# Optimization experiments

Hardware: AMD Instinct MI355X
Metric: run time of the kernel (lower is better)

## Reference

```python
import jax, jax.numpy as jnp
import numpy as np

B, C, H, W = 8, 256, 64, 64


def setup_inputs() -> dict:
    key = jax.random.key(0)
    ks = jax.random.split(key, 9)
    s = 1.0 / np.sqrt(C)  # conv2d default init scale
    return {
        "foreground": jax.random.normal(ks[0], (B, C, H, W), jnp.float32),
        "background": jax.random.normal(ks[1], (B, C, H, W), jnp.float32),
        "mask": jax.random.uniform(ks[2], (B, C, H, W), jnp.float32),
        "Wq": jax.random.normal(ks[3], (C, C), jnp.float32) * s,
        "bq": jnp.zeros((C,), jnp.float32),
        "Wk": jax.random.normal(ks[4], (C, C), jnp.float32) * s,
        "bk": jnp.zeros((C,), jnp.float32),
        "Wv": jax.random.normal(ks[5], (C, C), jnp.float32) * s,
        "bv": jnp.zeros((C,), jnp.float32),
        "gamma": jnp.ones((1,), jnp.float32),
    }


def _conv1x1(x, Wt, b):
    # 1x1 conv == per-pixel channel matmul; x: [B,C,H,W], Wt: [Cout,Cin]
    return jnp.einsum('bchw,oc->bohw', x, Wt) + b[None, :, None, None]


def reference(foreground, background, mask, Wq, bq, Wk, bk, Wv, bv, gamma):
    b, c, h, w = foreground.shape
    hw = h * w
    # mask is already at feature resolution (interpolate would be identity)
    q = _conv1x1(foreground, Wq, bq).reshape(b, c, hw)   # [B,C,HW]
    k = _conv1x1(background, Wk, bk).reshape(b, c, hw)   # [B,C,HW]
    # bmm(q, k^T): channel-channel correlation [B,C,C]
    corr = jnp.einsum('bci,bdi->bcd', q, k)
    m_r = mask.reshape(b, c, hw)                          # [B,C,HW]
    # bmm(corr, m_r): mask-modulated scores [B,C,HW]
    scores = jnp.einsum('bcd,bdi->bci', corr, m_r)
    energy = jax.nn.softmax(scores, axis=-1)
    v = _conv1x1(foreground, Wv, bv).reshape(b, c, hw)
    attended = (energy * v).reshape(b, c, h, w)
    out = foreground * mask + gamma[0] * (1.0 - mask) * attended
    return out
```

## Files before the change

### kernel.cpp

```cpp
#include <hip/hip_runtime.h>
#include <math.h>

#define B_    8
#define C_    256
#define HW_   4096
#define CHW_  ((long)C_ * HW_)

#define BKT   32
#define LDH   40
#define LDI   132
#define KS    16
#define KCH   (HW_ / KS)

typedef __attribute__((ext_vector_type(8))) short bf16x8;
typedef __attribute__((ext_vector_type(4))) float f32x4;
#define MFMA_BF16(a, b, c) __builtin_amdgcn_mfma_f32_16x16x32_bf16((a), (b), (c), 0, 0, 0)

union frag_u { uint4 u4; bf16x8 bf; };

__device__ __forceinline__ void cvt_hl4(const float4 f, uint* h, uint* l) {
    uint u0 = __float_as_uint(f.x), u1 = __float_as_uint(f.y),
         u2 = __float_as_uint(f.z), u3 = __float_as_uint(f.w);
    uint h0 = (u0 + 0x8000u) & 0xFFFF0000u, h1 = (u1 + 0x8000u) & 0xFFFF0000u,
         h2 = (u2 + 0x8000u) & 0xFFFF0000u, h3 = (u3 + 0x8000u) & 0xFFFF0000u;
    h[0] = (h0 >> 16) | h1;
    h[1] = (h2 >> 16) | h3;
    float l0 = f.x - __uint_as_float(h0), l1 = f.y - __uint_as_float(h1),
          l2 = f.z - __uint_as_float(h2), l3 = f.w - __uint_as_float(h3);
    uint a0 = __float_as_uint(l0) & 0xFFFF0000u, a1 = __float_as_uint(l1) & 0xFFFF0000u,
         a2 = __float_as_uint(l2) & 0xFFFF0000u, a3 = __float_as_uint(l3) & 0xFFFF0000u;
    l[0] = (a0 >> 16) | a1;
    l[1] = (a2 >> 16) | a3;
}
__device__ __forceinline__ void cvt_h4(const float4 f, uint* h) {
    uint u0 = __float_as_uint(f.x), u1 = __float_as_uint(f.y),
         u2 = __float_as_uint(f.z), u3 = __float_as_uint(f.w);
    uint h0 = (u0 + 0x8000u) & 0xFFFF0000u, h1 = (u1 + 0x8000u) & 0xFFFF0000u,
         h2 = (u2 + 0x8000u) & 0xFFFF0000u, h3 = (u3 + 0x8000u) & 0xFFFF0000u;
    h[0] = (h0 >> 16) | h1;
    h[1] = (h2 >> 16) | h3;
}

__device__ __forceinline__ void cvt8_hl(const float* f, bf16x8* bh, bf16x8* bl) {
    frag_u H, L;
    uint hw[8];
    #pragma unroll
    for (int j = 0; j < 4; ++j) {
        uint u0 = __float_as_uint(f[2*j]), u1 = __float_as_uint(f[2*j+1]);
        uint h0 = (u0 + 0x8000u) & 0xFFFF0000u;
        uint h1 = (u1 + 0x8000u) & 0xFFFF0000u;
        ((uint*)&H.u4)[j] = (h0 >> 16) | h1;
        hw[2*j] = h0; hw[2*j+1] = h1;
    }
    #pragma unroll
    for (int j = 0; j < 4; ++j) {
        float l0 = f[2*j]   - __uint_as_float(hw[2*j]);
        float l1 = f[2*j+1] - __uint_as_float(hw[2*j+1]);
        ((uint*)&L.u4)[j] = ((__float_as_uint(l0) & 0xFFFF0000u) >> 16)
                          |  (__float_as_uint(l1) & 0xFFFF0000u);
    }
    *bh = H.bf; *bl = L.bf;
}
__device__ __forceinline__ void cvt8_h(const float* f, bf16x8* bh) {
    frag_u H;
    #pragma unroll
    for (int j = 0; j < 4; ++j) {
        uint h0 = (__float_as_uint(f[2*j])   + 0x8000u) & 0xFFFF0000u;
        uint h1 = (__float_as_uint(f[2*j+1]) + 0x8000u) & 0xFFFF0000u;
        ((uint*)&H.u4)[j] = (h0 >> 16) | h1;
    }
    *bh = H.bf;
}

__global__ __launch_bounds__(256) void conv_w(
    const float* __restrict__ Wv, ushort* __restrict__ Wvh)
{
    const int i = (blockIdx.x * 256 + threadIdx.x) * 4;
    float4 v = *reinterpret_cast<const float4*>(&Wv[i]);
    uint h[2];
    cvt_h4(v, h);
    *reinterpret_cast<uint2*>(&Wvh[i]) = make_uint2(h[0], h[1]);
}

__global__ __launch_bounds__(256, 3) void gemm_nt_mfma(
    const float* __restrict__ F, const float* __restrict__ G,
    float* __restrict__ part,
    float* __restrict__ fsum, float* __restrict__ gsum)
{
    __shared__ ushort Ah[128 * LDH], Al[128 * LDH], Bh[128 * LDH], Bl[128 * LDH];

    const int z  = blockIdx.z;
    const int b  = z >> 4;
    const int ks = z & (KS - 1);
    const int c0 = blockIdx.y * 128;
    const int d0 = blockIdx.x * 128;
    const float* Fb = F + (long)b * CHW_ + (long)ks * KCH;
    const float* Gb = G + (long)b * CHW_ + (long)ks * KCH;
    const bool doF = (blockIdx.x == 0);
    const bool doG = (blockIdx.y == 0);

    const int t    = threadIdx.x;
    const int srow = t & 127;
    const int skf  = (t >> 7) * 16;
    const int lane = t & 63, w = t >> 6;
    const int col  = lane & 15, quad = lane >> 4;
    const int wm   = (w >> 1) * 64, wn = (w & 1) * 64;

    f32x4 acc[4][4] = {};
    float rsF = 0.0f, rsG = 0.0f;

    for (int kt = 0; kt < KCH; kt += BKT) {
        {
            const float* s = &Fb[(long)(c0 + srow) * HW_ + kt + skf];
            float4 v0 = *reinterpret_cast<const float4*>(s);
            float4 v1 = *reinterpret_cast<const float4*>(s + 4);
            float4 v2 = *reinterpret_cast<const float4*>(s + 8);
            float4 v3 = *reinterpret_cast<const float4*>(s + 12);
            if (doF) {
                rsF += (v0.x + v0.y + v0.z + v0.w) + (v1.x + v1.y + v1.z + v1.w)
                     + (v2.x + v2.y + v2.z + v2.w) + (v3.x + v3.y + v3.z + v3.w);
            }
            uint h[4], l[4];
            cvt_hl4(v0, h + 0, l + 0);
            cvt_hl4(v1, h + 2, l + 2);
            *reinterpret_cast<uint4*>(&Ah[srow * LDH + skf]) = make_uint4(h[0], h[1], h[2], h[3]);
            *reinterpret_cast<uint4*>(&Al[srow * LDH + skf]) = make_uint4(l[0], l[1], l[2], l[3]);
            cvt_hl4(v2, h + 0, l + 0);
            cvt_hl4(v3, h + 2, l + 2);
            *reinterpret_cast<uint4*>(&Ah[srow * LDH + skf + 8]) = make_uint4(h[0], h[1], h[2], h[3]);
            *reinterpret_cast<uint4*>(&Al[srow * LDH + skf + 8]) = make_uint4(l[0], l[1], l[2], l[3]);
        }
        {
            const float* s = &Gb[(long)(d0 + srow) * HW_ + kt + skf];
            float4 v0 = *reinterpret_cast<const float4*>(s);
            float4 v1 = *reinterpret_cast<const float4*>(s + 4);
            float4 v2 = *reinterpret_cast<const float4*>(s + 8);
            float4 v3 = *reinterpret_cast<const float4*>(s + 12);
            if (doG) {
                rsG += (v0.x + v0.y + v0.z + v0.w) + (v1.x + v1.y + v1.z + v1.w)
                     + (v2.x + v2.y + v2.z + v2.w) + (v3.x + v3.y + v3.z + v3.w);
            }
            uint h[4], l[4];
            cvt_hl4(v0, h + 0, l + 0);
            cvt_hl4(v1, h + 2, l + 2);
            *reinterpret_cast<uint4*>(&Bh[srow * LDH + skf]) = make_uint4(h[0], h[1], h[2], h[3]);
            *reinterpret_cast<uint4*>(&Bl[srow * LDH + skf]) = make_uint4(l[0], l[1], l[2], l[3]);
            cvt_hl4(v2, h + 0, l + 0);
            cvt_hl4(v3, h + 2, l + 2);
            *reinterpret_cast<uint4*>(&Bh[srow * LDH + skf + 8]) = make_uint4(h[0], h[1], h[2], h[3]);
            *reinterpret_cast<uint4*>(&Bl[srow * LDH + skf + 8]) = make_uint4(l[0], l[1], l[2], l[3]);
        }
        __syncthreads();

        bf16x8 bfh[4], bfl[4];
        #pragma unroll
        for (int tj = 0; tj < 4; ++tj) {
            const int r = (wn + tj * 16 + col) * LDH + quad * 8;
            bfh[tj] = *reinterpret_cast<const bf16x8*>(&Bh[r]);
            bfl[tj] = *reinterpret_cast<const bf16x8*>(&Bl[r]);
        }
        #pragma unroll
        for (int ti = 0; ti < 4; ++ti) {
            const int r = (wm + ti * 16 + col) * LDH + quad * 8;
            bf16x8 afh = *reinterpret_cast<const bf16x8*>(&Ah[r]);
            bf16x8 afl = *reinterpret_cast<const bf16x8*>(&Al[r]);
            #pragma unroll
            for (int tj = 0; tj < 4; ++tj) {
                acc[ti][tj] = MFMA_BF16(afh, bfh[tj], acc[ti][tj]);
                acc[ti][tj] = MFMA_BF16(afh, bfl[tj], acc[ti][tj]);
                acc[ti][tj] = MFMA_BF16(afl, bfh[tj], acc[ti][tj]);
            }
        }
        __syncthreads();
    }

    if (doF) atomicAdd(&fsum[b * C_ + c0 + srow], rsF);
    if (doG) atomicAdd(&gsum[b * C_ + d0 + srow], rsG);

    float* P = part + (long)z * C_ * C_;
    #pragma unroll
    for (int ti = 0; ti < 4; ++ti) {
        const int m = c0 + wm + ti * 16 + quad * 4;
        #pragma unroll
        for (int tj = 0; tj < 4; ++tj) {
            const int n = d0 + wn + tj * 16 + col;
            #pragma unroll
            for (int r = 0; r < 4; ++r)
                P[(long)(m + r) * C_ + n] = acc[ti][tj][r];
        }
    }
}

__global__ __launch_bounds__(256, 3) void gemm_stats_mfma(
    const ushort* __restrict__ corrh, const ushort* __restrict__ corrl,
    const float* __restrict__ mask,
    float* __restrict__ pmax, float* __restrict__ psum)
{
    __shared__ float Ms[32 * LDI];
    __shared__ float pm[2][128], ps[2][128];

    const int b  = blockIdx.z;
    const int m0 = blockIdx.y * 128;
    const int n0 = blockIdx.x * 128;
    const ushort* Ahb = corrh + (long)b * C_ * C_;
    const ushort* Alb = corrl + (long)b * C_ * C_;
    const float*  Mb  = mask + (long)b * CHW_;

    const int t    = threadIdx.x;
    const int se   = t >> 3;
    const int si4  = (t & 7) * 4;
    const int lane = t & 63, w = t >> 6;
    const int col  = lane & 15, quad = lane >> 4;
    const int wm   = (w >> 1) * 64, wn = (w & 1) * 64;

    f32x4 acc[4][4] = {};

    for (int kt = 0; kt < C_; kt += BKT) {
        __syncthreads();
        #pragma unroll
        for (int rep = 0; rep < 4; ++rep) {
            const int i = rep * 32 + si4;
            float4 v = *reinterpret_cast<const float4*>(&Mb[(long)(kt + se) * HW_ + n0 + i]);
            *reinterpret_cast<float4*>(&Ms[se * LDI + i]) = v;
        }
        __syncthreads();

        bf16x8 ah[4], al[4];
        #pragma unroll
        for (int ti = 0; ti < 4; ++ti) {
            const long oa = (long)(m0 + wm + ti * 16 + col) * C_ + kt + quad * 8;
            ah[ti] = *reinterpret_cast<const bf16x8*>(&Ahb[oa]);
            al[ti] = *reinterpret_cast<const bf16x8*>(&Alb[oa]);
        }
        #pragma unroll
        for (int tj = 0; tj < 4; ++tj) {
            const int i = wn + tj * 16 + col;
            float fv[8];
            #pragma unroll
            for (int j = 0; j < 8; ++j)
                fv[j] = Ms[(quad * 8 + j) * LDI + i];
            bf16x8 bh, bl;
            cvt8_hl(fv, &bh, &bl);
            #pragma unroll
            for (int ti = 0; ti < 4; ++ti) {
                acc[ti][tj] = MFMA_BF16(ah[ti], bh, acc[ti][tj]);
                acc[ti][tj] = MFMA_BF16(ah[ti], bl, acc[ti][tj]);
                acc[ti][tj] = MFMA_BF16(al[ti], bh, acc[ti][tj]);
            }
        }
    }

    #pragma unroll
    for (int ti = 0; ti < 4; ++ti) {
        #pragma unroll
        for (int r = 0; r < 4; ++r) {
            float mx = fmaxf(fmaxf(acc[ti][0][r], acc[ti][1][r]),
                             fmaxf(acc[ti][2][r], acc[ti][3][r]));
            mx = fmaxf(mx, __shfl_xor(mx, 1));
            mx = fmaxf(mx, __shfl_xor(mx, 2));
            mx = fmaxf(mx, __shfl_xor(mx, 4));
            mx = fmaxf(mx, __shfl_xor(mx, 8));
            float se2 = __expf(acc[ti][0][r] - mx) + __expf(acc[ti][1][r] - mx)
                      + __expf(acc[ti][2][r] - mx) + __expf(acc[ti][3][r] - mx);
            se2 += __shfl_xor(se2, 1);
            se2 += __shfl_xor(se2, 2);
            se2 += __shfl_xor(se2, 4);
            se2 += __shfl_xor(se2, 8);
            if (col == 0) {
                const int rb = wm + ti * 16 + quad * 4 + r;
                pm[w & 1][rb] = mx;
                ps[w & 1][rb] = se2;
            }
        }
    }
    __syncthreads();
    if (t < 128) {
        const float a0 = pm[0][t], a1 = pm[1][t];
        const float gm = fmaxf(a0, a1);
        const float gs = ps[0][t] * __expf(a0 - gm) + ps[1][t] * __expf(a1 - gm);
        const long rowg = (long)b * C_ + m0 + t;
        pmax[rowg * 32 + blockIdx.x] = gm;
        psum[rowg * 32 + blockIdx.x] = gs;
    }
}

__global__ __launch_bounds__(256, 2) void gemm_fused_final(
    const ushort* __restrict__ corrh, const ushort* __restrict__ corrl,
    const ushort* __restrict__ Wvh,
    const float* __restrict__ mask,   const float* __restrict__ fg,
    const float* __restrict__ pmax,   const float* __restrict__ psum,
    const float* __restrict__ bv,     const float* __restrict__ gamma,
    float* __restrict__ out)
{
    __shared__ float Ms[32 * LDI];
    __shared__ float Fs[32 * LDI];
    __shared__ float sm[128], si[128];

    const int b  = blockIdx.z;
    const int m0 = blockIdx.y * 128;
    const int n0 = blockIdx.x * 128;
    const ushort* Ahb = corrh + (long)b * C_ * C_;
    const ushort* Alb = corrl + (long)b * C_ * C_;
    const float*  Mb  = mask + (long)b * CHW_;
    const float*  Fgb = fg   + (long)b * CHW_;

    const int t    = threadIdx.x;
    const int se   = t >> 3;
    const int si4  = (t & 7) * 4;
    const int lane = t & 63, w = t >> 6;
    const int col  = lane & 15, quad = lane >> 4;
    const int wm   = (w >> 1) * 64, wn = (w & 1) * 64;

    if (t < 128) {
        const long rowg = (long)b * C_ + m0 + t;
        const float* pmr = pmax + rowg * 32;
        const float* psr = psum + rowg * 32;
        float gm = -INFINITY;
        #pragma unroll
        for (int i = 0; i < 32; ++i) gm = fmaxf(gm, pmr[i]);
        float gs = 0.0f;
        #pragma unroll
        for (int i = 0; i < 32; ++i) gs += psr[i] * __expf(pmr[i] - gm);
        sm[t] = gm;
        si[t] = 1.0f / gs;
    }

    f32x4 acc_s[4][4] = {};
    f32x4 acc_v[4][4] = {};

    for (int kt = 0; kt < C_; kt += BKT) {
        __syncthreads();
        #pragma unroll
        for (int rep = 0; rep < 4; ++rep) {
            const int i = rep * 32 + si4;
            float4 vm = *reinterpret_cast<const float4*>(&Mb[(long)(kt + se) * HW_ + n0 + i]);
            float4 vf = *reinterpret_cast<const float4*>(&Fgb[(long)(kt + se) * HW_ + n0 + i]);
            *reinterpret_cast<float4*>(&Ms[se * LDI + i]) = vm;
            *reinterpret_cast<float4*>(&Fs[se * LDI + i]) = vf;
        }
        __syncthreads();

        bf16x8 ah[4], al[4], aw[4];
        #pragma unroll
        for (int ti = 0; ti < 4; ++ti) {
            const long oa = (long)(m0 + wm + ti * 16 + col) * C_ + kt + quad * 8;
            ah[ti] = *reinterpret_cast<const bf16x8*>(&Ahb[oa]);
            al[ti] = *reinterpret_cast<const bf16x8*>(&Alb[oa]);
            aw[ti] = *reinterpret_cast<const bf16x8*>(&Wvh[oa]);
        }
        #pragma unroll
        for (int tj = 0; tj < 4; ++tj) {
            const int i = wn + tj * 16 + col;
            float fv[8], gv[8];
            #pragma unroll
            for (int j = 0; j < 8; ++j) {
                fv[j] = Ms[(quad * 8 + j) * LDI + i];
                gv[j] = Fs[(quad * 8 + j) * LDI + i];
            }
            bf16x8 bh, bl, bf;
            cvt8_hl(fv, &bh, &bl);
            cvt8_h(gv, &bf);
            #pragma unroll
            for (int ti = 0; ti < 4; ++ti) {
                acc_s[ti][tj] = MFMA_BF16(ah[ti], bh, acc_s[ti][tj]);
                acc_s[ti][tj] = MFMA_BF16(ah[ti], bl, acc_s[ti][tj]);
                acc_s[ti][tj] = MFMA_BF16(al[ti], bh, acc_s[ti][tj]);
                acc_v[ti][tj] = MFMA_BF16(aw[ti], bf, acc_v[ti][tj]);
            }
        }
    }

    const float g = gamma[0];
    #pragma unroll
    for (int ti = 0; ti < 4; ++ti) {
        #pragma unroll
        for (int r = 0; r < 4; ++r) {
            const int lrow = wm + ti * 16 + quad * 4 + r;
            const float mx  = sm[lrow];
            const float inv = si[lrow] * g;
            #pragma unroll
            for (int tj = 0; tj < 4; ++tj)
                acc_s[ti][tj][r] = __expf(acc_s[ti][tj][r] - mx) * inv;
        }
    }

    #pragma unroll
    for (int ti = 0; ti < 4; ++ti) {
        const int m = m0 + wm + ti * 16 + quad * 4;
        #pragma unroll
        for (int r = 0; r < 4; ++r) {
            const float bvm = bv[m + r];
            #pragma unroll
            for (int tj = 0; tj < 4; ++tj) {
                const int n = n0 + wn + tj * 16 + col;
                const long e = (long)b * CHW_ + (long)(m + r) * HW_ + n;
                const float f  = fg[e];
                const float mk = mask[e];
                const float vv = acc_v[ti][tj][r] + bvm;
                out[e] = f * mk + (1.0f - mk) * acc_s[ti][tj][r] * vv;
            }
        }
    }
}

__global__ __launch_bounds__(256) void reduce_part(
    const float* __restrict__ part, float* __restrict__ S1)
{
    const long idx = (long)blockIdx.x * 256 + threadIdx.x;
    const int  b   = (int)(idx >> 16);
    const long e   = idx & 65535;
    const float* p = part + ((long)b * KS) * 65536 + e;
    float s = 0.0f;
    #pragma unroll
    for (int ks = 0; ks < KS; ++ks) s += p[(long)ks * 65536];
    S1[idx] = s;
}

#define BK64 16
#define LDT64 68
__global__ __launch_bounds__(256) void gemm_nt64(
    const float* __restrict__ S1, const float* __restrict__ Wk,
    float* __restrict__ T)
{
    __shared__ float As[BK64][LDT64];
    __shared__ float Bs[BK64][LDT64];
    const int r0 = blockIdx.y * 64;
    const int d0 = blockIdx.x * 64;
    const int t   = threadIdx.x;
    const int tx  = t & 15, ty = t >> 4;
    const int tx4 = tx * 4, ty4 = ty * 4;
    const int am  = t >> 2, ak4 = (t & 3) * 4;

    float acc[4][4] = {};
    for (int k0 = 0; k0 < C_; k0 += BK64) {
        float4 av = *reinterpret_cast<const float4*>(&S1[(long)(r0 + am) * C_ + k0 + ak4]);
        float4 bw = *reinterpret_cast<const float4*>(&Wk[(long)(d0 + am) * C_ + k0 + ak4]);
        As[ak4+0][am]=av.x; As[ak4+1][am]=av.y; As[ak4+2][am]=av.z; As[ak4+3][am]=av.w;
        Bs[ak4+0][am]=bw.x; Bs[ak4+1][am]=bw.y; Bs[ak4+2][am]=bw.z; Bs[ak4+3][am]=bw.w;
        __syncthreads();
        #pragma unroll
        for (int kk = 0; kk < BK64; ++kk) {
            float4 a = *reinterpret_cast<const float4*>(&As[kk][ty4]);
            float4 x = *reinterpret_cast<const float4*>(&Bs[kk][tx4]);
            const float ar[4] = {a.x,a.y,a.z,a.w};
            const float xr[4] = {x.x,x.y,x.z,x.w};
            #pragma unroll
            for (int r = 0; r < 4; ++r)
                #pragma unroll
                for (int s = 0; s < 4; ++s)
                    acc[r][s] = fmaf(ar[r], xr[s], acc[r][s]);
        }
        __syncthreads();
    }
    #pragma unroll
    for (int r = 0; r < 4; ++r) {
        float4 o; o.x=acc[r][0]; o.y=acc[r][1]; o.z=acc[r][2]; o.w=acc[r][3];
        *reinterpret_cast<float4*>(&T[(long)(r0 + ty4 + r) * C_ + d0 + tx4]) = o;
    }
}

__global__ __launch_bounds__(256) void gemm_nn64_rank1(
    const float* __restrict__ Wq, const float* __restrict__ T,
    const float* __restrict__ Wk, const float* __restrict__ bk,
    const float* __restrict__ bq,
    const float* __restrict__ fsum, const float* __restrict__ gsum,
    ushort* __restrict__ corrh, ushort* __restrict__ corrl)
{
    __shared__ float As[BK64][LDT64];
    __shared__ float Bs[BK64][LDT64];
    __shared__ float u_s[64], wh_s[64];
    const int b  = blockIdx.z;
    const int m0 = blockIdx.y * 64;
    const int n0 = blockIdx.x * 64;
    const float* Tb = T + (long)b * C_ * C_;

    const int t   = threadIdx.x;
    const int tx  = t & 15, ty = t >> 4;
    const int tx4 = tx * 4, ty4 = ty * 4;
    const int am  = t >> 2, ak4 = (t & 3) * 4;
    const int xk  = ty,     xn4 = tx4;

    if (t < 64) {
        const float* wrow = Wq + (long)(m0 + t) * C_;
        const float* s = fsum + b * C_;
        float a = 0.0f;
        for (int e2 = 0; e2 < C_; ++e2) a = fmaf(wrow[e2], s[e2], a);
        u_s[t] = a;
    } else if (t < 128) {
        const int d = n0 + (t - 64);
        const float* wrow = Wk + (long)d * C_;
        const float* s = gsum + b * C_;
        float a = 0.0f;
        for (int e2 = 0; e2 < C_; ++e2) a = fmaf(wrow[e2], s[e2], a);
        wh_s[t - 64] = a + (float)HW_ * bk[d];
    }

    float acc[4][4] = {};
    for (int k0 = 0; k0 < C_; k0 += BK64) {
        float4 av = *reinterpret_cast<const float4*>(&Wq[(long)(m0 + am) * C_ + k0 + ak4]);
        float4 xv = *reinterpret_cast<const float4*>(&Tb[(long)(k0 + xk) * C_ + n0 + xn4]);
        As[ak4+0][am]=av.x; As[ak4+1][am]=av.y; As[ak4+2][am]=av.z; As[ak4+3][am]=av.w;
        *reinterpret_cast<float4*>(&Bs[xk][xn4]) = xv;
        __syncthreads();
        #pragma unroll
        for (int kk = 0; kk < BK64; ++kk) {
            float4 a = *reinterpret_cast<const float4*>(&As[kk][ty4]);
            float4 x = *reinterpret_cast<const float4*>(&Bs[kk][tx4]);
            const float ar[4] = {a.x,a.y,a.z,a.w};
            const float xr[4] = {x.x,x.y,x.z,x.w};
            #pragma unroll
            for (int r = 0; r < 4; ++r)
                #pragma unroll
                for (int s = 0; s < 4; ++s)
                    acc[r][s] = fmaf(ar[r], xr[s], acc[r][s]);
        }
        __syncthreads();
    }

    float4 bkv = *reinterpret_cast<const float4*>(&bk[n0 + tx4]);
    float4 whv = make_float4(wh_s[tx4], wh_s[tx4+1], wh_s[tx4+2], wh_s[tx4+3]);
    #pragma unroll
    for (int r = 0; r < 4; ++r) {
        const int m = m0 + ty4 + r;
        const float um = u_s[ty4 + r];
        const float bm = bq[m];
        float4 o;
        o.x = acc[r][0] + um*bkv.x + bm*whv.x;
        o.y = acc[r][1] + um*bkv.y + bm*whv.y;
        o.z = acc[r][2] + um*bkv.z + bm*whv.z;
        o.w = acc[r][3] + um*bkv.w + bm*whv.w;
        uint h[2], l[2];
        cvt_hl4(o, h, l);
        const long e = (long)b * C_ * C_ + (long)m * C_ + n0 + tx4;
        *reinterpret_cast<uint2*>(&corrh[e]) = make_uint2(h[0], h[1]);
        *reinterpret_cast<uint2*>(&corrl[e]) = make_uint2(l[0], l[1]);
    }
}

extern "C" void kernel_launch(void* const* d_in, const int* in_sizes, int n_in,
                              void* d_out, int out_size, void* d_ws, size_t ws_size,
                              hipStream_t stream)
{
    const float* fg    = (const float*)d_in[0];
    const float* bg    = (const float*)d_in[1];
    const float* mask  = (const float*)d_in[2];
    const float* Wq    = (const float*)d_in[3];
    const float* bq    = (const float*)d_in[4];
    const float* Wk    = (const float*)d_in[5];
    const float* bk    = (const float*)d_in[6];
    const float* Wv    = (const float*)d_in[7];
    const float* bv    = (const float*)d_in[8];
    const float* gamma = (const float*)d_in[9];
    float* out = (float*)d_out;

    char* ws = (char*)d_ws;
    float*  part   = (float*)(ws);
    float*  S1     = (float*)(ws + 33554432);
    float*  T      = (float*)(ws + 35651584);
    ushort* corrh  = (ushort*)(ws + 37748736);
    ushort* corrl  = (ushort*)(ws + 38797312);
    ushort* Wvh    = (ushort*)(ws + 39845888);
    float*  fsum   = (float*)(ws + 39976960);
    float*  gsum   = (float*)(ws + 39985152);
    float*  pmax   = (float*)(ws + 39993344);
    float*  psum   = (float*)(ws + 40255488);

    const dim3 blk(256);

    hipMemsetAsync(fsum, 0, 16384, stream);

    conv_w<<<dim3(64), blk, 0, stream>>>(Wv, Wvh);

    gemm_nt_mfma<<<dim3(2, 2, B_ * KS), blk, 0, stream>>>(fg, bg, part, fsum, gsum);
    reduce_part<<<dim3(B_ * C_ * C_ / 256), blk, 0, stream>>>(part, S1);

    gemm_nt64<<<dim3(C_ / 64, B_ * C_ / 64), blk, 0, stream>>>(S1, Wk, T);
    gemm_nn64_rank1<<<dim3(4, 4, B_), blk, 0, stream>>>(
        Wq, T, Wk, bk, bq, fsum, gsum, corrh, corrl);

    gemm_stats_mfma<<<dim3(HW_ / 128, C_ / 128, B_), blk, 0, stream>>>(
        corrh, corrl, mask, pmax, psum);

    gemm_fused_final<<<dim3(HW_ / 128, C_ / 128, B_), blk, 0, stream>>>(
        corrh, corrl, Wvh, mask, fg, pmax, psum, bv, gamma, out);
}
```

Measured before the change: 277.5 us.

## Pre-transpose and convert mask and foreground to split bf16 for direct MFMA loads

Adds a transpose_cvt kernel that writes mask (high and low bf16 parts) and foreground (high bf16 part) in a [B,HW,C] layout once. The stats and fused-final GEMMs then load MFMA B fragments straight from global memory instead of staging fp32 tiles in shared memory and converting them per block with barriers. This removes the repeated conversion and the LDS traffic from two kernels. In exchange it adds an extra pass that writes about 48MB of bf16 data, and the GEMMs now read uncached, strided global fragments without LDS reuse. The new buffers reuse the partial-sum workspace region.

```diff
diff --git a/kernel.cpp b/kernel.cpp
--- a/kernel.cpp
+++ b/kernel.cpp
@@ -8,7 +8,6 @@
 
 #define BKT   32
 #define LDH   40
-#define LDI   132
 #define KS    16
 #define KCH   (HW_ / KS)
 
@@ -41,35 +40,17 @@
     h[1] = (h2 >> 16) | h3;
 }
 
-__device__ __forceinline__ void cvt8_hl(const float* f, bf16x8* bh, bf16x8* bl) {
-    frag_u H, L;
-    uint hw[8];
-    #pragma unroll
-    for (int j = 0; j < 4; ++j) {
-        uint u0 = __float_as_uint(f[2*j]), u1 = __float_as_uint(f[2*j+1]);
-        uint h0 = (u0 + 0x8000u) & 0xFFFF0000u;
-        uint h1 = (u1 + 0x8000u) & 0xFFFF0000u;
-        ((uint*)&H.u4)[j] = (h0 >> 16) | h1;
-        hw[2*j] = h0; hw[2*j+1] = h1;
-    }
-    #pragma unroll
-    for (int j = 0; j < 4; ++j) {
-        float l0 = f[2*j]   - __uint_as_float(hw[2*j]);
-        float l1 = f[2*j+1] - __uint_as_float(hw[2*j+1]);
-        ((uint*)&L.u4)[j] = ((__float_as_uint(l0) & 0xFFFF0000u) >> 16)
-                          |  (__float_as_uint(l1) & 0xFFFF0000u);
-    }
-    *bh = H.bf; *bl = L.bf;
-}
-__device__ __forceinline__ void cvt8_h(const float* f, bf16x8* bh) {
-    frag_u H;
-    #pragma unroll
-    for (int j = 0; j < 4; ++j) {
-        uint h0 = (__float_as_uint(f[2*j])   + 0x8000u) & 0xFFFF0000u;
-        uint h1 = (__float_as_uint(f[2*j+1]) + 0x8000u) & 0xFFFF0000u;
-        ((uint*)&H.u4)[j] = (h0 >> 16) | h1;
-    }
-    *bh = H.bf;
+__device__ __forceinline__ void cvt2_hl(float a, float b2, uint* h, uint* l) {
+    uint ua = __float_as_uint(a), ub = __float_as_uint(b2);
+    uint ha = (ua + 0x8000u) & 0xFFFF0000u, hb = (ub + 0x8000u) & 0xFFFF0000u;
+    *h = (ha >> 16) | hb;
+    float la = a - __uint_as_float(ha), lb = b2 - __uint_as_float(hb);
+    *l = ((__float_as_uint(la) & 0xFFFF0000u) >> 16) | (__float_as_uint(lb) & 0xFFFF0000u);
+}
+__device__ __forceinline__ uint cvt2_h(float a, float b2) {
+    uint ha = (__float_as_uint(a) + 0x8000u) & 0xFFFF0000u;
+    uint hb = (__float_as_uint(b2) + 0x8000u) & 0xFFFF0000u;
+    return (ha >> 16) | hb;
 }
 
 __global__ __launch_bounds__(256) void conv_w(
@@ -80,6 +61,47 @@
     uint h[2];
     cvt_h4(v, h);
     *reinterpret_cast<uint2*>(&Wvh[i]) = make_uint2(h[0], h[1]);
+}
+
+__global__ __launch_bounds__(256) void transpose_cvt(
+    const float* __restrict__ mask, const float* __restrict__ fg,
+    ushort* __restrict__ mTh, ushort* __restrict__ mTl, ushort* __restrict__ fTh)
+{
+    __shared__ float Ms[64][65];
+    __shared__ float Fs[64][65];
+
+    const int b  = blockIdx.z;
+    const int c0 = blockIdx.y * 64;
+    const int i0 = blockIdx.x * 64;
+    const int t  = threadIdx.x;
+
+    const int lr = t >> 2;
+    const int lc = (t & 3) * 16;
+    const float* mp = mask + (long)b * CHW_ + (long)(c0 + lr) * HW_ + i0 + lc;
+    const float* fp = fg   + (long)b * CHW_ + (long)(c0 + lr) * HW_ + i0 + lc;
+    #pragma unroll
+    for (int j = 0; j < 16; j += 4) {
+        *reinterpret_cast<float4*>(&Ms[lr][lc + j]) = *reinterpret_cast<const float4*>(mp + j);
+        *reinterpret_cast<float4*>(&Fs[lr][lc + j]) = *reinterpret_cast<const float4*>(fp + j);
+    }
+    __syncthreads();
+
+    const int oi = t >> 2;
+    const int oc = (t & 3) * 16;
+    uint hm[8], lm[8], hf[8];
+    #pragma unroll
+    for (int j = 0; j < 8; ++j) {
+        const float m0v = Ms[oc + 2 * j][oi], m1v = Ms[oc + 2 * j + 1][oi];
+        cvt2_hl(m0v, m1v, &hm[j], &lm[j]);
+        hf[j] = cvt2_h(Fs[oc + 2 * j][oi], Fs[oc + 2 * j + 1][oi]);
+    }
+    const long ro = ((long)b * HW_ + i0 + oi) * C_ + c0 + oc;
+    *reinterpret_cast<uint4*>(&mTh[ro])     = make_uint4(hm[0], hm[1], hm[2], hm[3]);
+    *reinterpret_cast<uint4*>(&mTh[ro + 8]) = make_uint4(hm[4], hm[5], hm[6], hm[7]);
+    *reinterpret_cast<uint4*>(&mTl[ro])     = make_uint4(lm[0], lm[1], lm[2], lm[3]);
+    *reinterpret_cast<uint4*>(&mTl[ro + 8]) = make_uint4(lm[4], lm[5], lm[6], lm[7]);
+    *reinterpret_cast<uint4*>(&fTh[ro])     = make_uint4(hf[0], hf[1], hf[2], hf[3]);
+    *reinterpret_cast<uint4*>(&fTh[ro + 8]) = make_uint4(hf[4], hf[5], hf[6], hf[7]);
 }
 
 __global__ __launch_bounds__(256, 3) void gemm_nt_mfma(
@@ -191,12 +213,11 @@
     }
 }
 
-__global__ __launch_bounds__(256, 3) void gemm_stats_mfma(
+__global__ __launch_bounds__(256, 2) void gemm_stats_mfma(
     const ushort* __restrict__ corrh, const ushort* __restrict__ corrl,
-    const float* __restrict__ mask,
+    const ushort* __restrict__ mTh,   const ushort* __restrict__ mTl,
     float* __restrict__ pmax, float* __restrict__ psum)
 {
-    __shared__ float Ms[32 * LDI];
     __shared__ float pm[2][128], ps[2][128];
 
     const int b  = blockIdx.z;
@@ -204,28 +225,19 @@
     const int n0 = blockIdx.x * 128;
     const ushort* Ahb = corrh + (long)b * C_ * C_;
     const ushort* Alb = corrl + (long)b * C_ * C_;
-    const float*  Mb  = mask + (long)b * CHW_;
+    const ushort* Bhb = mTh + (long)b * HW_ * C_;
+    const ushort* Blb = mTl + (long)b * HW_ * C_;
 
     const int t    = threadIdx.x;
-    const int se   = t >> 3;
-    const int si4  = (t & 7) * 4;
     const int lane = t & 63, w = t >> 6;
     const int col  = lane & 15, quad = lane >> 4;
     const int wm   = (w >> 1) * 64, wn = (w & 1) * 64;
 
     f32x4 acc[4][4] = {};
 
+    #pragma unroll 1
     for (int kt = 0; kt < C_; kt += BKT) {
-        __syncthreads();
-        #pragma unroll
-        for (int rep = 0; rep < 4; ++rep) {
-            const int i = rep * 32 + si4;
-            float4 v = *reinterpret_cast<const float4*>(&Mb[(long)(kt + se) * HW_ + n0 + i]);
-            *reinterpret_cast<float4*>(&Ms[se * LDI + i]) = v;
-        }
-        __syncthreads();
-
-        bf16x8 ah[4], al[4];
+        bf16x8 ah[4], al[4], bh[4], bl[4];
         #pragma unroll
         for (int ti = 0; ti < 4; ++ti) {
             const long oa = (long)(m0 + wm + ti * 16 + col) * C_ + kt + quad * 8;
@@ -234,18 +246,17 @@
         }
         #pragma unroll
         for (int tj = 0; tj < 4; ++tj) {
-            const int i = wn + tj * 16 + col;
-            float fv[8];
-            #pragma unroll
-            for (int j = 0; j < 8; ++j)
-                fv[j] = Ms[(quad * 8 + j) * LDI + i];
-            bf16x8 bh, bl;
-            cvt8_hl(fv, &bh, &bl);
+            const long ob = (long)(n0 + wn + tj * 16 + col) * C_ + kt + quad * 8;
+            bh[tj] = *reinterpret_cast<const bf16x8*>(&Bhb[ob]);
+            bl[tj] = *reinterpret_cast<const bf16x8*>(&Blb[ob]);
+        }
+        #pragma unroll
+        for (int tj = 0; tj < 4; ++tj) {
             #pragma unroll
             for (int ti = 0; ti < 4; ++ti) {
-                acc[ti][tj] = MFMA_BF16(ah[ti], bh, acc[ti][tj]);
-                acc[ti][tj] = MFMA_BF16(ah[ti], bl, acc[ti][tj]);
-                acc[ti][tj] = MFMA_BF16(al[ti], bh, acc[ti][tj]);
+                acc[ti][tj] = MFMA_BF16(ah[ti], bh[tj], acc[ti][tj]);
+                acc[ti][tj] = MFMA_BF16(ah[ti], bl[tj], acc[ti][tj]);
+                acc[ti][tj] = MFMA_BF16(al[ti], bh[tj], acc[ti][tj]);
             }
         }
     }
@@ -287,13 +298,13 @@
 __global__ __launch_bounds__(256, 2) void gemm_fused_final(
     const ushort* __restrict__ corrh, const ushort* __restrict__ corrl,
     const ushort* __restrict__ Wvh,
+    const ushort* __restrict__ mTh,   const ushort* __restrict__ mTl,
+    const ushort* __restrict__ fTh,
     const float* __restrict__ mask,   const float* __restrict__ fg,
     const float* __restrict__ pmax,   const float* __restrict__ psum,
     const float* __restrict__ bv,     const float* __restrict__ gamma,
     float* __restrict__ out)
 {
-    __shared__ float Ms[32 * LDI];
-    __shared__ float Fs[32 * LDI];
     __shared__ float sm[128], si[128];
 
     const int b  = blockIdx.z;
@@ -301,12 +312,11 @@
     const int n0 = blockIdx.x * 128;
     const ushort* Ahb = corrh + (long)b * C_ * C_;
     const ushort* Alb = corrl + (long)b * C_ * C_;
-    const float*  Mb  = mask + (long)b * CHW_;
-    const float*  Fgb = fg   + (long)b * CHW_;
+    const ushort* Bhb = mTh + (long)b * HW_ * C_;
+    const ushort* Blb = mTl + (long)b * HW_ * C_;
+    const ushort* Bfb = fTh + (long)b * HW_ * C_;
 
     const int t    = threadIdx.x;
-    const int se   = t >> 3;
-    const int si4  = (t & 7) * 4;
     const int lane = t & 63, w = t >> 6;
     const int col  = lane & 15, quad = lane >> 4;
     const int wm   = (w >> 1) * 64, wn = (w & 1) * 64;
@@ -328,19 +338,9 @@
     f32x4 acc_s[4][4] = {};
     f32x4 acc_v[4][4] = {};
 
+    #pragma unroll 1
     for (int kt = 0; kt < C_; kt += BKT) {
-        __syncthreads();
-        #pragma unroll
-        for (int rep = 0; rep < 4; ++rep) {
-            const int i = rep * 32 + si4;
-            float4 vm = *reinterpret_cast<const float4*>(&Mb[(long)(kt + se) * HW_ + n0 + i]);
-            float4 vf = *reinterpret_cast<const float4*>(&Fgb[(long)(kt + se) * HW_ + n0 + i]);
-            *reinterpret_cast<float4*>(&Ms[se * LDI + i]) = vm;
-            *reinterpret_cast<float4*>(&Fs[se * LDI + i]) = vf;
-        }
-        __syncthreads();
-
-        bf16x8 ah[4], al[4], aw[4];
+        bf16x8 ah[4], al[4], aw[4], bh[4], bl[4], bf[4];
         #pragma unroll
         for (int ti = 0; ti < 4; ++ti) {
             const long oa = (long)(m0 + wm + ti * 16 + col) * C_ + kt + quad * 8;
@@ -350,25 +350,24 @@
         }
         #pragma unroll
         for (int tj = 0; tj < 4; ++tj) {
-            const int i = wn + tj * 16 + col;
-            float fv[8], gv[8];
-            #pragma unroll
-            for (int j = 0; j < 8; ++j) {
-                fv[j] = Ms[(quad * 8 + j) * LDI + i];
-                gv[j] = Fs[(quad * 8 + j) * LDI + i];
-            }
-            bf16x8 bh, bl, bf;
-            cvt8_hl(fv, &bh, &bl);
-            cvt8_h(gv, &bf);
+            const long ob = (long)(n0 + wn + tj * 16 + col) * C_ + kt + quad * 8;
+            bh[tj] = *reinterpret_cast<const bf16x8*>(&Bhb[ob]);
+            bl[tj] = *reinterpret_cast<const bf16x8*>(&Blb[ob]);
+            bf[tj] = *reinterpret_cast<const bf16x8*>(&Bfb[ob]);
+        }
+        #pragma unroll
+        for (int tj = 0; tj < 4; ++tj) {
             #pragma unroll
             for (int ti = 0; ti < 4; ++ti) {
-                acc_s[ti][tj] = MFMA_BF16(ah[ti], bh, acc_s[ti][tj]);
-                acc_s[ti][tj] = MFMA_BF16(ah[ti], bl, acc_s[ti][tj]);
-                acc_s[ti][tj] = MFMA_BF16(al[ti], bh, acc_s[ti][tj]);
-                acc_v[ti][tj] = MFMA_BF16(aw[ti], bf, acc_v[ti][tj]);
-            }
-        }
-    }
+                acc_s[ti][tj] = MFMA_BF16(ah[ti], bh[tj], acc_s[ti][tj]);
+                acc_s[ti][tj] = MFMA_BF16(ah[ti], bl[tj], acc_s[ti][tj]);
+                acc_s[ti][tj] = MFMA_BF16(al[ti], bh[tj], acc_s[ti][tj]);
+                acc_v[ti][tj] = MFMA_BF16(aw[ti], bf[tj], acc_v[ti][tj]);
+            }
+        }
+    }
+
+    __syncthreads();
 
     const float g = gamma[0];
     #pragma unroll
@@ -564,6 +563,9 @@
     float*  gsum   = (float*)(ws + 39985152);
     float*  pmax   = (float*)(ws + 39993344);
     float*  psum   = (float*)(ws + 40255488);
+    ushort* mTh    = (ushort*)(ws);
+    ushort* mTl    = (ushort*)(ws + 16777216);
+    ushort* fTh    = (ushort*)(ws + 40517632);
 
     const dim3 blk(256);
 
@@ -573,14 +575,17 @@
 
     gemm_nt_mfma<<<dim3(2, 2, B_ * KS), blk, 0, stream>>>(fg, bg, part, fsum, gsum);
     reduce_part<<<dim3(B_ * C_ * C_ / 256), blk, 0, stream>>>(part, S1);
+
+    transpose_cvt<<<dim3(HW_ / 64, C_ / 64, B_), blk, 0, stream>>>(
+        mask, fg, mTh, mTl, fTh);
 
     gemm_nt64<<<dim3(C_ / 64, B_ * C_ / 64), blk, 0, stream>>>(S1, Wk, T);
     gemm_nn64_rank1<<<dim3(4, 4, B_), blk, 0, stream>>>(
         Wq, T, Wk, bk, bq, fsum, gsum, corrh, corrl);
 
     gemm_stats_mfma<<<dim3(HW_ / 128, C_ / 128, B_), blk, 0, stream>>>(
-        corrh, corrl, mask, pmax, psum);
+        corrh, corrl, mTh, mTl, pmax, psum);
 
     gemm_fused_final<<<dim3(HW_ / 128, C_ / 128, B_), blk, 0, stream>>>(
-        corrh, corrl, Wvh, mask, fg, pmax, psum, bv, gamma, out);
-}
+        corrh, corrl, Wvh, mTh, mTl, fTh, mask, fg, pmax, psum, bv, gamma, out);
+}
```

Measured after the change: 324.7 us. +17.0%, slower.
